# Optimization experiments

Measured on AMD Instinct MI355X. Metric: run time of the kernel, lower is better.

Reference implementation:

```python
import jax, jax.numpy as jnp
import numpy as np

B, S, D, H, L, DFF = 16, 256, 768, 12, 6, 2048
IMG, P, C = 256, 16, 3
HD = D // H
EPS = 1e-5


def _n(k, shp, scale=0.02):
    return jax.random.normal(k, shp, jnp.float32) * scale


def setup_inputs() -> dict:
    key = jax.random.key(0)
    ks = jax.random.split(key, 9)
    return dict(
        encoded_patches=jax.random.normal(ks[0], (B, S, D), jnp.float32),
        W_self_in=_n(ks[1], (L, 3 * D, D)), b_self_in=jnp.zeros((L, 3 * D), jnp.float32),
        W_self_out=_n(ks[2], (L, D, D)), b_self_out=jnp.zeros((L, D), jnp.float32),
        W_cross_in=_n(ks[3], (L, 3 * D, D)), b_cross_in=jnp.zeros((L, 3 * D), jnp.float32),
        W_cross_out=_n(ks[4], (L, D, D)), b_cross_out=jnp.zeros((L, D), jnp.float32),
        ln1_g=jnp.ones((L, D), jnp.float32), ln1_b=jnp.zeros((L, D), jnp.float32),
        ln2_g=jnp.ones((L, D), jnp.float32), ln2_b=jnp.zeros((L, D), jnp.float32),
        ln3_g=jnp.ones((L, D), jnp.float32), ln3_b=jnp.zeros((L, D), jnp.float32),
        W_ff1=_n(ks[5], (L, DFF, D)), b_ff1=jnp.zeros((L, DFF), jnp.float32),
        W_ff2=_n(ks[6], (L, D, DFF)), b_ff2=jnp.zeros((L, D), jnp.float32),
        W_patch=_n(ks[7], (C * P * P, D)), b_patch=jnp.zeros((C * P * P,), jnp.float32),
    )


def sinusoidal_pe(seq, d):
    pos = jnp.arange(seq, dtype=jnp.float32)[:, None]
    div = jnp.exp(jnp.arange(0, d, 2, dtype=jnp.float32) * (-np.log(10000.0) / d))
    pe = jnp.zeros((seq, d), jnp.float32)
    pe = pe.at[:, 0::2].set(jnp.sin(pos * div))
    pe = pe.at[:, 1::2].set(jnp.cos(pos * div))
    return pe


def layer_norm(x, g, b):
    mu = x.mean(-1, keepdims=True)
    var = ((x - mu) ** 2).mean(-1, keepdims=True)
    return (x - mu) * jax.lax.rsqrt(var + EPS) * g + b


def mha(q_in, kv_in, W_in, b_in, W_out, b_out, mask):
    # W_in: [3D, D] packed q,k,v (PyTorch in_proj layout); Linear: y = x W^T + b
    Wq, Wk, Wv = jnp.split(W_in, 3, axis=0)
    bq, bk, bv = jnp.split(b_in, 3, axis=0)
    Bq = q_in.shape[0]
    q = (q_in @ Wq.T + bq).reshape(Bq, -1, H, HD)
    k = (kv_in @ Wk.T + bk).reshape(Bq, -1, H, HD)
    v = (kv_in @ Wv.T + bv).reshape(Bq, -1, H, HD)
    scores = jnp.einsum('bqhd,bkhd->bhqk', q, k) / np.sqrt(HD)
    if mask is not None:
        scores = scores + mask  # mask broadcasts [S, S] with -inf above diag
    attn = jax.nn.softmax(scores, axis=-1)
    out = jnp.einsum('bhqk,bkhd->bqhd', attn, v).reshape(Bq, -1, D)
    return out @ W_out.T + b_out


def reference(encoded_patches, W_self_in, b_self_in, W_self_out, b_self_out,
              W_cross_in, b_cross_in, W_cross_out, b_cross_out,
              ln1_g, ln1_b, ln2_g, ln2_b, ln3_g, ln3_b,
              W_ff1, b_ff1, W_ff2, b_ff2, W_patch, b_patch):
    # The original loops over growing prefixes i=1..S and takes the last
    # position each time. With a causal self-attn mask and per-position
    # cross-attn/FFN/LN, that is mathematically identical to one full
    # causal pass; we compute it once. (eval mode: dropout = identity)
    pe = sinusoidal_pe(S, D)
    causal = jnp.where(jnp.triu(jnp.ones((S, S), jnp.float32), 1) > 0, -jnp.inf, 0.0)
    mem = encoded_patches
    x = encoded_patches + pe[None, :, :]
    for l in range(L):
        # post-norm TransformerDecoderLayer (PyTorch default norm_first=False)
        x = layer_norm(x + mha(x, x, W_self_in[l], b_self_in[l],
                               W_self_out[l], b_self_out[l], causal),
                       ln1_g[l], ln1_b[l])
        x = layer_norm(x + mha(x, mem, W_cross_in[l], b_cross_in[l],
                               W_cross_out[l], b_cross_out[l], None),
                       ln2_g[l], ln2_b[l])
        ff = jax.nn.relu(x @ W_ff1[l].T + b_ff1[l]) @ W_ff2[l].T + b_ff2[l]
        x = layer_norm(x + ff, ln3_g[l], ln3_b[l])
    out = x @ W_patch.T + b_patch                       # [B, S, C*P*P]
    out = out.reshape(-1, IMG, IMG, C)                  # naive view, as in source
    return jnp.transpose(out, (0, 3, 1, 2))             # [B, C, IMG, IMG]
```

## Files before the change

### kernel.cpp

```cpp
#include <hip/hip_runtime.h>
#include <hip/hip_bf16.h>

#define DEV __device__ __forceinline__

typedef __bf16 bf16x8 __attribute__((ext_vector_type(8)));
typedef __bf16 bf16x4 __attribute__((ext_vector_type(4)));
typedef float  f32x4  __attribute__((ext_vector_type(4)));

DEV bf16x8 cvt8(const float4 a, const float4 b) {
    bf16x8 r;
    r[0] = (__bf16)a.x; r[1] = (__bf16)a.y; r[2] = (__bf16)a.z; r[3] = (__bf16)a.w;
    r[4] = (__bf16)b.x; r[5] = (__bf16)b.y; r[6] = (__bf16)b.z; r[7] = (__bf16)b.w;
    return r;
}

DEV void gload_lds16(const __bf16* g, __bf16* l) {
    __builtin_amdgcn_global_load_lds(
        (const __attribute__((address_space(1))) void*)g,
        (__attribute__((address_space(3))) void*)l, 16, 0, 0);
}

DEV void wconv_one(const float* __restrict__ src, __bf16* __restrict__ dst,
                   int lg, int gpr, int K) {
    const int n = lg / gpr;
    const int gi = lg - n * gpr;
    const int cb = (gi >> 3) << 6;
    const int g = gi & 7;
    const float* sp = src + (size_t)n * K + cb + ((g ^ (n & 7)) << 3);
    float4 a = *(const float4*)sp;
    float4 b = *(const float4*)(sp + 4);
    *(bf16x8*)&dst[(size_t)lg * 8] = cvt8(a, b);
}

__global__ __launch_bounds__(256) void wconv(const float* __restrict__ W,
                                             __bf16* __restrict__ Wb) {
    const int gid = blockIdx.x * 256 + threadIdx.x;
    wconv_one(W, Wb, gid, 96, 768);
}

__global__ __launch_bounds__(256) void wconv4(const float* __restrict__ s0,
                                              const float* __restrict__ s1,
                                              const float* __restrict__ s2,
                                              const float* __restrict__ s3,
                                              __bf16* __restrict__ dst) {
    const int gid = blockIdx.x * 256 + threadIdx.x;
    if (gid < 221184)      wconv_one(s0, dst,           gid,          96, 768);
    else if (gid < 294912) wconv_one(s1, dst + 1769472, gid - 221184, 96, 768);
    else if (gid < 516096) wconv_one(s2, dst + 2359296, gid - 294912, 96, 768);
    else                   wconv_one(s3, dst + 4128768, gid - 516096, 96, 768);
}

__global__ __launch_bounds__(256) void wconv_ff(const float* __restrict__ f1,
                                                const float* __restrict__ f2,
                                                __bf16* __restrict__ dst) {
    const int gid = blockIdx.x * 256 + threadIdx.x;
    if (gid < 196608) wconv_one(f1, dst,           gid,          96, 768);
    else              wconv_one(f2, dst + 1572864, gid - 196608, 256, 2048);
}

__global__ __launch_bounds__(256) void cvt_lin(const float* __restrict__ in,
                                               __bf16* __restrict__ out) {
    const int g = blockIdx.x * 256 + threadIdx.x;
    float4 a = *(const float4*)(in + g * 8);
    float4 b = *(const float4*)(in + g * 8 + 4);
    *(bf16x8*)&out[g * 8] = cvt8(a, b);
}

template <int RELU, int OUT_BF16, int BN>
__global__ __launch_bounds__(256) void gemm_bt(const __bf16* __restrict__ Xb,
                                               const __bf16* __restrict__ Wb,
                                               const float* __restrict__ bias,
                                               float* __restrict__ Yf,
                                               __bf16* __restrict__ Yb,
                                               int ldy, int K) {
    __shared__ __bf16 As[128 * 64];
    __shared__ __bf16 Bs[BN * 64];

    const int tid = threadIdx.x;
    const int lane = tid & 63;
    const int wave = tid >> 6;
    constexpr int NI = (BN == 128) ? 4 : 2;
    const int wr = (BN == 128) ? (wave >> 1) : wave;
    const int wc = (BN == 128) ? (wave & 1) : 0;
    const int lr = lane & 15;

    const int mBase = blockIdx.y * 128;
    const int nBase = blockIdx.x * BN;

    const int ar = tid >> 3;
    const int ap = tid & 7;
    const __bf16* Ab = Xb + (size_t)mBase * K + ap * 8;

    const int brow = lane >> 3;
    const __bf16* Bb = Wb + (size_t)nBase * K + (lane & 7) * 8;

    f32x4 acc[NI][4];
#pragma unroll
    for (int i = 0; i < NI; ++i)
#pragma unroll
        for (int j = 0; j < 4; ++j) {
            f32x4 z = {0.f, 0.f, 0.f, 0.f};
            acc[i][j] = z;
        }

    for (int kt = 0; kt < K; kt += 64) {
#pragma unroll
        for (int i = 0; i < 4; ++i) {
            const int row = i * 32 + ar;
            bf16x8 v = *(const bf16x8*)(Ab + (size_t)row * K + kt);
            *(bf16x8*)&As[row * 64 + ((ap ^ (row & 7)) << 3)] = v;
        }
#pragma unroll
        for (int i = 0; i < BN / 32; ++i) {
            const int r0 = wave * (BN / 4) + i * 8;
            gload_lds16(Bb + (size_t)(r0 + brow) * K + kt, &Bs[r0 * 64]);
        }
        __syncthreads();
#pragma unroll
        for (int kk = 0; kk < 2; ++kk) {
            const int q = (lane >> 4) + kk * 4;
            bf16x8 af[NI], bfv[4];
#pragma unroll
            for (int i = 0; i < NI; ++i) {
                const int r = wr * (NI * 16) + i * 16 + lr;
                af[i] = *(const bf16x8*)&As[r * 64 + ((q ^ (r & 7)) << 3)];
            }
#pragma unroll
            for (int j = 0; j < 4; ++j) {
                const int r = wc * 64 + j * 16 + lr;
                bfv[j] = *(const bf16x8*)&Bs[r * 64 + ((q ^ (r & 7)) << 3)];
            }
#pragma unroll
            for (int i = 0; i < NI; ++i)
#pragma unroll
                for (int j = 0; j < 4; ++j)
                    acc[i][j] = __builtin_amdgcn_mfma_f32_16x16x32_bf16(af[i], bfv[j], acc[i][j], 0, 0, 0);
        }
        __syncthreads();
    }

    const int rsub = (lane >> 4) << 2;
#pragma unroll
    for (int i = 0; i < NI; ++i)
#pragma unroll
        for (int j = 0; j < 4; ++j) {
            const int col = nBase + wc * 64 + j * 16 + lr;
            const float bv = bias[col];
#pragma unroll
            for (int rr = 0; rr < 4; ++rr) {
                const int row = mBase + wr * (NI * 16) + i * 16 + rsub + rr;
                float v = acc[i][j][rr] + bv;
                if (RELU) v = fmaxf(v, 0.f);
                if (OUT_BF16) Yb[(size_t)row * ldy + col] = (__bf16)v;
                else          Yf[(size_t)row * ldy + col] = v;
            }
        }
}

__global__ __launch_bounds__(256) void attn_mfma(const __bf16* __restrict__ QKV,
                                                 __bf16* __restrict__ Oout,
                                                 int causal) {
    const int bh = blockIdx.x;
    const int qq = blockIdx.y;
    const int b = bh / 12, h = bh - b * 12;
    const int tid = threadIdx.x;
    const int lane = tid & 63;
    const int w = tid >> 6;
    const int g = lane >> 4;
    const int c = lane & 15;
    const int c7 = c & 7;

    __shared__ __bf16 Ks[64 * 64];
    __shared__ __bf16 Vs[64 * 66];
    __shared__ __bf16 Ps[64 * 64];

    const int q64 = (w << 4) + c;
    const int qrow = (qq << 6) + q64;
    const __bf16* qp = QKV + (size_t)((b << 8) + qrow) * 2304 + (h << 6) + (g << 3);
    bf16x8 qf0 = *(const bf16x8*)qp;
    bf16x8 qf1 = *(const bf16x8*)(qp + 32);

    f32x4 oacc[4];
#pragma unroll
    for (int i = 0; i < 4; ++i) { f32x4 z = {0.f, 0.f, 0.f, 0.f}; oacc[i] = z; }
    float mrun = -1e30f, lrun = 0.f;

    const int nt = causal ? (qq + 1) : 4;
    const int sr = tid >> 2;
    const int sg0 = (tid & 3) << 1;
    const int sp = sg0 << 3;

    for (int kt = 0; kt < nt; ++kt) {
        __syncthreads();
        {
            const __bf16* kp = QKV + (size_t)((b << 8) + (kt << 6) + sr) * 2304 + 768 + (h << 6) + sp;
            bf16x8 k0 = *(const bf16x8*)kp;
            bf16x8 k1 = *(const bf16x8*)(kp + 8);
            bf16x8 v0 = *(const bf16x8*)(kp + 768);
            bf16x8 v1 = *(const bf16x8*)(kp + 776);
            const int s7 = sr & 7;
            *(bf16x8*)&Ks[(sr << 6) + ((sg0 ^ s7) << 3)] = k0;
            *(bf16x8*)&Ks[(sr << 6) + (((sg0 + 1) ^ s7) << 3)] = k1;
            uint32_t* vd = (uint32_t*)&Vs[sr * 66 + sp];
            const uint32_t* u0 = (const uint32_t*)&v0;
            const uint32_t* u1 = (const uint32_t*)&v1;
            vd[0] = u0[0]; vd[1] = u0[1]; vd[2] = u0[2]; vd[3] = u0[3];
            vd[4] = u1[0]; vd[5] = u1[1]; vd[6] = u1[2]; vd[7] = u1[3];
        }
        __syncthreads();

        f32x4 sc[4];
#pragma unroll
        for (int mf = 0; mf < 4; ++mf) { f32x4 z = {0.f, 0.f, 0.f, 0.f}; sc[mf] = z; }
#pragma unroll
        for (int mf = 0; mf < 4; ++mf) {
            const int row = (mf << 4) + c;
            bf16x8 af0 = *(const bf16x8*)&Ks[(row << 6) + ((g ^ c7) << 3)];
            sc[mf] = __builtin_amdgcn_mfma_f32_16x16x32_bf16(af0, qf0, sc[mf], 0, 0, 0);
            bf16x8 af1 = *(const bf16x8*)&Ks[(row << 6) + (((g + 4) ^ c7) << 3)];
            sc[mf] = __builtin_amdgcn_mfma_f32_16x16x32_bf16(af1, qf1, sc[mf], 0, 0, 0);
        }

        const int diag = (causal && kt == qq);
        float tm = -1e30f;
#pragma unroll
        for (int mf = 0; mf < 4; ++mf)
#pragma unroll
            for (int r = 0; r < 4; ++r) {
                float v = sc[mf][r] * 0.125f;
                if (diag && ((mf << 4) + (g << 2) + r > q64)) v = -1e30f;
                sc[mf][r] = v;
                tm = fmaxf(tm, v);
            }
        tm = fmaxf(tm, __shfl_xor(tm, 16));
        tm = fmaxf(tm, __shfl_xor(tm, 32));
        const float mnew = fmaxf(mrun, tm);
        const float rs = __expf(mrun - mnew);
        mrun = mnew;
        lrun *= rs;
#pragma unroll
        for (int i = 0; i < 4; ++i) {
            oacc[i][0] *= rs; oacc[i][1] *= rs; oacc[i][2] *= rs; oacc[i][3] *= rs;
        }

#pragma unroll
        for (int mf = 0; mf < 4; ++mf) {
            const int kg = (mf << 1) + (g >> 1);
            const int e = (g & 1) << 2;
#pragma unroll
            for (int r = 0; r < 4; ++r) {
                float p = __expf(sc[mf][r] - mnew);
                lrun += p;
                Ps[(q64 << 6) + ((kg ^ c7) << 3) + e + r] = (__bf16)p;
            }
        }

#pragma unroll
        for (int kc = 0; kc < 2; ++kc) {
            bf16x8 pb = *(const bf16x8*)&Ps[(q64 << 6) + (((g + (kc << 2)) ^ c7) << 3)];
#pragma unroll
            for (int df = 0; df < 4; ++df) {
                bf16x8 av;
#pragma unroll
                for (int j = 0; j < 8; ++j)
                    av[j] = Vs[((g << 3) + j + (kc << 5)) * 66 + (df << 4) + c];
                oacc[df] = __builtin_amdgcn_mfma_f32_16x16x32_bf16(av, pb, oacc[df], 0, 0, 0);
            }
        }
    }

    lrun += __shfl_xor(lrun, 16);
    lrun += __shfl_xor(lrun, 32);
    const float inv = 1.f / lrun;
    __bf16* op = Oout + (size_t)((b << 8) + qrow) * 768 + (h << 6) + (g << 2);
#pragma unroll
    for (int df = 0; df < 4; ++df) {
        bf16x4 ov;
        ov[0] = (__bf16)(oacc[df][0] * inv);
        ov[1] = (__bf16)(oacc[df][1] * inv);
        ov[2] = (__bf16)(oacc[df][2] * inv);
        ov[3] = (__bf16)(oacc[df][3] * inv);
        *(bf16x4*)(op + (df << 4)) = ov;
    }
}

__global__ __launch_bounds__(256) void resid_ln(float* __restrict__ x,
                                                __bf16* __restrict__ xb,
                                                const float* __restrict__ r,
                                                const float* __restrict__ g,
                                                const float* __restrict__ b) {
    const int row = blockIdx.x, tid = threadIdx.x;
    float* xp = x + (size_t)row * 768;
    __bf16* xbp = xb + (size_t)row * 768;
    const float* rp = r + (size_t)row * 768;

    float v0 = xp[tid] + rp[tid];
    float v1 = xp[tid + 256] + rp[tid + 256];
    float v2 = xp[tid + 512] + rp[tid + 512];

    __shared__ float red[4];
    float s = v0 + v1 + v2;
#pragma unroll
    for (int off = 32; off > 0; off >>= 1) s += __shfl_down(s, off, 64);
    if ((tid & 63) == 0) red[tid >> 6] = s;
    __syncthreads();
    const float mean = (red[0] + red[1] + red[2] + red[3]) * (1.0f / 768.0f);
    __syncthreads();

    float d0 = v0 - mean, d1 = v1 - mean, d2 = v2 - mean;
    float q = d0 * d0 + d1 * d1 + d2 * d2;
#pragma unroll
    for (int off = 32; off > 0; off >>= 1) q += __shfl_down(q, off, 64);
    if ((tid & 63) == 0) red[tid >> 6] = q;
    __syncthreads();
    const float inv = rsqrtf((red[0] + red[1] + red[2] + red[3]) * (1.0f / 768.0f) + 1e-5f);

    const float o0 = d0 * inv * g[tid] + b[tid];
    const float o1 = d1 * inv * g[tid + 256] + b[tid + 256];
    const float o2 = d2 * inv * g[tid + 512] + b[tid + 512];
    xp[tid] = o0;       xbp[tid] = (__bf16)o0;
    xp[tid + 256] = o1; xbp[tid + 256] = (__bf16)o1;
    xp[tid + 512] = o2; xbp[tid + 512] = (__bf16)o2;
}

__global__ __launch_bounds__(256) void add_pe(const float* __restrict__ e,
                                              float* __restrict__ x,
                                              __bf16* __restrict__ xb) {
    const int i = blockIdx.x * 256 + threadIdx.x;
    const int m = i / 768;
    const int d = i - m * 768;
    const int s = m & 255;
    const int pair = d >> 1;
    const float div = __expf((float)(2 * pair) * (-0.011992630693328381f));
    const float ang = (float)s * div;
    const float pe = (d & 1) ? cosf(ang) : sinf(ang);
    const float v = e[i] + pe;
    x[i] = v;
    xb[i] = (__bf16)v;
}

__global__ __launch_bounds__(256) void write_out(const float* __restrict__ p, float* __restrict__ o) {
    const int i = blockIdx.x * 256 + threadIdx.x;
    const int m = i / 768;
    const int j = i - m * 768;
    const int b = m >> 8, s = m & 255;
    const int w = j / 3;
    const int c = j - w * 3;
    o[(size_t)b * 196608 + (size_t)c * 65536 + s * 256 + w] = p[i];
}

extern "C" void kernel_launch(void* const* d_in, const int* in_sizes, int n_in,
                              void* d_out, int out_size, void* d_ws, size_t ws_size,
                              hipStream_t stream) {
    const float* enc         = (const float*)d_in[0];
    const float* W_self_in   = (const float*)d_in[1];
    const float* b_self_in   = (const float*)d_in[2];
    const float* W_self_out  = (const float*)d_in[3];
    const float* b_self_out  = (const float*)d_in[4];
    const float* W_cross_in  = (const float*)d_in[5];
    const float* b_cross_in  = (const float*)d_in[6];
    const float* W_cross_out = (const float*)d_in[7];
    const float* b_cross_out = (const float*)d_in[8];
    const float* ln1_g       = (const float*)d_in[9];
    const float* ln1_b       = (const float*)d_in[10];
    const float* ln2_g       = (const float*)d_in[11];
    const float* ln2_b       = (const float*)d_in[12];
    const float* ln3_g       = (const float*)d_in[13];
    const float* ln3_b       = (const float*)d_in[14];
    const float* W_ff1       = (const float*)d_in[15];
    const float* b_ff1       = (const float*)d_in[16];
    const float* W_ff2       = (const float*)d_in[17];
    const float* b_ff2       = (const float*)d_in[18];
    const float* W_patch     = (const float*)d_in[19];
    const float* b_patch     = (const float*)d_in[20];

    float* out = (float*)d_out;
    float* ws  = (float*)d_ws;

    float*  x       = ws;
    __bf16* xb      = (__bf16*)(ws + 3145728);
    __bf16* qkvb    = (__bf16*)(ws + 4718592);
    __bf16* attnout = (__bf16*)(ws + 9437184);
    float*  proj    = ws + 11010048;
    __bf16* encb    = (__bf16*)(ws + 14155776);
    __bf16* wbuf    = (__bf16*)(ws + 15728640);

    add_pe<<<12288, 256, 0, stream>>>(enc, x, xb);
    cvt_lin<<<1536, 256, 0, stream>>>(enc, encb);

    for (int l = 0; l < 6; ++l) {
        const float* Wsi = W_self_in   + (size_t)l * 2304 * 768;
        const float* Wso = W_self_out  + (size_t)l * 768 * 768;
        const float* Wci = W_cross_in  + (size_t)l * 2304 * 768;
        const float* Wco = W_cross_out + (size_t)l * 768 * 768;
        const float* Wf1 = W_ff1       + (size_t)l * 2048 * 768;
        const float* Wf2 = W_ff2       + (size_t)l * 768 * 2048;

        wconv4<<<2304, 256, 0, stream>>>(Wsi, Wso, Wci, Wco, wbuf);

        gemm_bt<0, 1, 128><<<dim3(18, 32), 256, 0, stream>>>(xb, wbuf, b_self_in + l * 2304,
                                                             nullptr, qkvb, 2304, 768);
        attn_mfma<<<dim3(192, 4), 256, 0, stream>>>(qkvb, attnout, 1);
        gemm_bt<0, 0, 64><<<dim3(12, 32), 256, 0, stream>>>(attnout, wbuf + 1769472,
                                                            b_self_out + l * 768,
                                                            proj, nullptr, 768, 768);
        resid_ln<<<4096, 256, 0, stream>>>(x, xb, proj, ln1_g + l * 768, ln1_b + l * 768);

        gemm_bt<0, 1, 64><<<dim3(12, 32), 256, 0, stream>>>(xb, wbuf + 2359296,
                                                            b_cross_in + l * 2304,
                                                            nullptr, qkvb, 2304, 768);
        gemm_bt<0, 1, 128><<<dim3(12, 32), 256, 0, stream>>>(encb, wbuf + 2949120,
                                                             b_cross_in + l * 2304 + 768,
                                                             nullptr, qkvb + 768, 2304, 768);
        attn_mfma<<<dim3(192, 4), 256, 0, stream>>>(qkvb, attnout, 0);
        gemm_bt<0, 0, 64><<<dim3(12, 32), 256, 0, stream>>>(attnout, wbuf + 4128768,
                                                            b_cross_out + l * 768,
                                                            proj, nullptr, 768, 768);
        resid_ln<<<4096, 256, 0, stream>>>(x, xb, proj, ln2_g + l * 768, ln2_b + l * 768);

        wconv_ff<<<1536, 256, 0, stream>>>(Wf1, Wf2, wbuf);
        gemm_bt<1, 1, 128><<<dim3(16, 32), 256, 0, stream>>>(xb, wbuf, b_ff1 + l * 2048,
                                                             nullptr, qkvb, 2048, 768);
        gemm_bt<0, 0, 64><<<dim3(12, 32), 256, 0, stream>>>(qkvb, wbuf + 1572864,
                                                            b_ff2 + l * 768,
                                                            proj, nullptr, 768, 2048);
        resid_ln<<<4096, 256, 0, stream>>>(x, xb, proj, ln3_g + l * 768, ln3_b + l * 768);
    }

    wconv<<<288, 256, 0, stream>>>(W_patch, wbuf);
    gemm_bt<0, 0, 64><<<dim3(12, 32), 256, 0, stream>>>(xb, wbuf, b_patch,
                                                        proj, nullptr, 768, 768);
    write_out<<<12288, 256, 0, stream>>>(proj, out);
}
```

Measured before the change: 1.486 ms.

## Pre-swizzle bf16 activations so GEMM A-tiles load directly into LDS

Producers of bf16 activations (layer norm, embedding, GEMM bf16 epilogue, attention output) now write rows in the XOR-swizzled layout the GEMM expects. The GEMM can then load A tiles with direct global-to-LDS loads, and attention can load K the same way. The change also remaps block IDs across 8 groups for cache locality, fuses the enc conversion into add_pe, vectorises add_pe with fast sin/cos, and writes the final output permutation straight from the GEMM epilogue, removing the write_out kernel. The risk is that every consumer must agree on the swizzle, and the fast sin/cos intrinsics lower accuracy slightly.

```diff
diff --git a/kernel.cpp b/kernel.cpp
--- a/kernel.cpp
+++ b/kernel.cpp
@@ -18,6 +18,10 @@
     __builtin_amdgcn_global_load_lds(
         (const __attribute__((address_space(1))) void*)g,
         (__attribute__((address_space(3))) void*)l, 16, 0, 0);
+}
+
+DEV int swzcol(int col, int row) {
+    return (col & ~63) | ((((col >> 3) & 7) ^ (row & 7)) << 3) | (col & 7);
 }
 
 DEV void wconv_one(const float* __restrict__ src, __bf16* __restrict__ dst,
@@ -58,15 +62,7 @@
     else              wconv_one(f2, dst + 1572864, gid - 196608, 256, 2048);
 }
 
-__global__ __launch_bounds__(256) void cvt_lin(const float* __restrict__ in,
-                                               __bf16* __restrict__ out) {
-    const int g = blockIdx.x * 256 + threadIdx.x;
-    float4 a = *(const float4*)(in + g * 8);
-    float4 b = *(const float4*)(in + g * 8 + 4);
-    *(bf16x8*)&out[g * 8] = cvt8(a, b);
-}
-
-template <int RELU, int OUT_BF16, int BN>
+template <int RELU, int OUT, int BN>
 __global__ __launch_bounds__(256) void gemm_bt(const __bf16* __restrict__ Xb,
                                                const __bf16* __restrict__ Wb,
                                                const float* __restrict__ bias,
@@ -84,15 +80,18 @@
     const int wc = (BN == 128) ? (wave & 1) : 0;
     const int lr = lane & 15;
 
-    const int mBase = blockIdx.y * 128;
-    const int nBase = blockIdx.x * BN;
-
-    const int ar = tid >> 3;
-    const int ap = tid & 7;
-    const __bf16* Ab = Xb + (size_t)mBase * K + ap * 8;
+    const int nx = gridDim.x;
+    int bid = blockIdx.y * nx + blockIdx.x;
+    const int cpx = (nx * gridDim.y) >> 3;
+    bid = (bid & 7) * cpx + (bid >> 3);
+    const int by = bid / nx;
+    const int bx = bid - by * nx;
+    const int mBase = by * 128;
+    const int nBase = bx * BN;
 
     const int brow = lane >> 3;
-    const __bf16* Bb = Wb + (size_t)nBase * K + (lane & 7) * 8;
+    const __bf16* Ap = Xb + (size_t)mBase * K + ((lane & 7) << 3);
+    const __bf16* Bp = Wb + (size_t)nBase * K + ((lane & 7) << 3);
 
     f32x4 acc[NI][4];
 #pragma unroll
@@ -106,29 +105,28 @@
     for (int kt = 0; kt < K; kt += 64) {
 #pragma unroll
         for (int i = 0; i < 4; ++i) {
-            const int row = i * 32 + ar;
-            bf16x8 v = *(const bf16x8*)(Ab + (size_t)row * K + kt);
-            *(bf16x8*)&As[row * 64 + ((ap ^ (row & 7)) << 3)] = v;
+            const int r0 = (wave << 5) + (i << 3);
+            gload_lds16(Ap + (size_t)(r0 + brow) * K + kt, &As[r0 << 6]);
         }
 #pragma unroll
         for (int i = 0; i < BN / 32; ++i) {
-            const int r0 = wave * (BN / 4) + i * 8;
-            gload_lds16(Bb + (size_t)(r0 + brow) * K + kt, &Bs[r0 * 64]);
+            const int r0 = wave * (BN / 4) + (i << 3);
+            gload_lds16(Bp + (size_t)(r0 + brow) * K + kt, &Bs[r0 << 6]);
         }
         __syncthreads();
 #pragma unroll
         for (int kk = 0; kk < 2; ++kk) {
-            const int q = (lane >> 4) + kk * 4;
+            const int q = (lane >> 4) + (kk << 2);
             bf16x8 af[NI], bfv[4];
 #pragma unroll
             for (int i = 0; i < NI; ++i) {
                 const int r = wr * (NI * 16) + i * 16 + lr;
-                af[i] = *(const bf16x8*)&As[r * 64 + ((q ^ (r & 7)) << 3)];
+                af[i] = *(const bf16x8*)&As[(r << 6) + ((q ^ (r & 7)) << 3)];
             }
 #pragma unroll
             for (int j = 0; j < 4; ++j) {
                 const int r = wc * 64 + j * 16 + lr;
-                bfv[j] = *(const bf16x8*)&Bs[r * 64 + ((q ^ (r & 7)) << 3)];
+                bfv[j] = *(const bf16x8*)&Bs[(r << 6) + ((q ^ (r & 7)) << 3)];
             }
 #pragma unroll
             for (int i = 0; i < NI; ++i)
@@ -151,8 +149,15 @@
                 const int row = mBase + wr * (NI * 16) + i * 16 + rsub + rr;
                 float v = acc[i][j][rr] + bv;
                 if (RELU) v = fmaxf(v, 0.f);
-                if (OUT_BF16) Yb[(size_t)row * ldy + col] = (__bf16)v;
-                else          Yf[(size_t)row * ldy + col] = v;
+                if (OUT == 1) {
+                    Yb[(size_t)row * ldy + swzcol(col, row)] = (__bf16)v;
+                } else if (OUT == 2) {
+                    const int b_ = row >> 8, s_ = row & 255;
+                    const int w_ = col / 3, c_ = col - w_ * 3;
+                    Yf[(size_t)b_ * 196608 + (size_t)c_ * 65536 + s_ * 256 + w_] = v;
+                } else {
+                    Yf[(size_t)row * ldy + col] = v;
+                }
             }
         }
 }
@@ -172,13 +177,12 @@
 
     __shared__ __bf16 Ks[64 * 64];
     __shared__ __bf16 Vs[64 * 66];
-    __shared__ __bf16 Ps[64 * 64];
 
     const int q64 = (w << 4) + c;
     const int qrow = (qq << 6) + q64;
-    const __bf16* qp = QKV + (size_t)((b << 8) + qrow) * 2304 + (h << 6) + (g << 3);
-    bf16x8 qf0 = *(const bf16x8*)qp;
-    bf16x8 qf1 = *(const bf16x8*)(qp + 32);
+    const __bf16* qp = QKV + (size_t)((b << 8) + qrow) * 2304 + (h << 6);
+    bf16x8 qf0 = *(const bf16x8*)(qp + ((g ^ c7) << 3));
+    bf16x8 qf1 = *(const bf16x8*)(qp + (((g + 4) ^ c7) << 3));
 
     f32x4 oacc[4];
 #pragma unroll
@@ -193,19 +197,24 @@
     for (int kt = 0; kt < nt; ++kt) {
         __syncthreads();
         {
-            const __bf16* kp = QKV + (size_t)((b << 8) + (kt << 6) + sr) * 2304 + 768 + (h << 6) + sp;
-            bf16x8 k0 = *(const bf16x8*)kp;
-            bf16x8 k1 = *(const bf16x8*)(kp + 8);
-            bf16x8 v0 = *(const bf16x8*)(kp + 768);
-            bf16x8 v1 = *(const bf16x8*)(kp + 776);
+            const __bf16* Kp = QKV + (size_t)((b << 8) + (kt << 6)) * 2304 + 768 + (h << 6) + ((lane & 7) << 3);
+#pragma unroll
+            for (int i = 0; i < 2; ++i) {
+                const int r0 = (w << 4) + (i << 3);
+                gload_lds16(Kp + (size_t)(r0 + (lane >> 3)) * 2304, &Ks[r0 << 6]);
+            }
+        }
+        {
+            const __bf16* vp = QKV + (size_t)((b << 8) + (kt << 6) + sr) * 2304 + 1536 + (h << 6);
+            bf16x8 v0 = *(const bf16x8*)(vp + sp);
+            bf16x8 v1 = *(const bf16x8*)(vp + sp + 8);
             const int s7 = sr & 7;
-            *(bf16x8*)&Ks[(sr << 6) + ((sg0 ^ s7) << 3)] = k0;
-            *(bf16x8*)&Ks[(sr << 6) + (((sg0 + 1) ^ s7) << 3)] = k1;
-            uint32_t* vd = (uint32_t*)&Vs[sr * 66 + sp];
+            uint32_t* d0 = (uint32_t*)&Vs[sr * 66 + ((sg0 ^ s7) << 3)];
+            uint32_t* d1 = (uint32_t*)&Vs[sr * 66 + (((sg0 + 1) ^ s7) << 3)];
             const uint32_t* u0 = (const uint32_t*)&v0;
             const uint32_t* u1 = (const uint32_t*)&v1;
-            vd[0] = u0[0]; vd[1] = u0[1]; vd[2] = u0[2]; vd[3] = u0[3];
-            vd[4] = u1[0]; vd[5] = u1[1]; vd[6] = u1[2]; vd[7] = u1[3];
+            d0[0] = u0[0]; d0[1] = u0[1]; d0[2] = u0[2]; d0[3] = u0[3];
+            d1[0] = u1[0]; d1[1] = u1[1]; d1[2] = u1[2]; d1[3] = u1[3];
         }
         __syncthreads();
 
@@ -243,6 +252,7 @@
             oacc[i][0] *= rs; oacc[i][1] *= rs; oacc[i][2] *= rs; oacc[i][3] *= rs;
         }
 
+        __shared__ __bf16 Ps[64 * 64];
 #pragma unroll
         for (int mf = 0; mf < 4; ++mf) {
             const int kg = (mf << 1) + (g >> 1);
@@ -272,7 +282,7 @@
     lrun += __shfl_xor(lrun, 16);
     lrun += __shfl_xor(lrun, 32);
     const float inv = 1.f / lrun;
-    __bf16* op = Oout + (size_t)((b << 8) + qrow) * 768 + (h << 6) + (g << 2);
+    __bf16* op = Oout + (size_t)((b << 8) + qrow) * 768 + (h << 6);
 #pragma unroll
     for (int df = 0; df < 4; ++df) {
         bf16x4 ov;
@@ -280,7 +290,8 @@
         ov[1] = (__bf16)(oacc[df][1] * inv);
         ov[2] = (__bf16)(oacc[df][2] * inv);
         ov[3] = (__bf16)(oacc[df][3] * inv);
-        *(bf16x4*)(op + (df << 4)) = ov;
+        const int gran = (df << 1) + (g >> 1);
+        *(bf16x4*)(op + ((gran ^ c7) << 3) + ((g & 1) << 2)) = ov;
     }
 }
 
@@ -318,35 +329,43 @@
     const float o0 = d0 * inv * g[tid] + b[tid];
     const float o1 = d1 * inv * g[tid + 256] + b[tid + 256];
     const float o2 = d2 * inv * g[tid + 512] + b[tid + 512];
-    xp[tid] = o0;       xbp[tid] = (__bf16)o0;
-    xp[tid + 256] = o1; xbp[tid + 256] = (__bf16)o1;
-    xp[tid + 512] = o2; xbp[tid + 512] = (__bf16)o2;
+    xp[tid] = o0;       xbp[swzcol(tid, row)] = (__bf16)o0;
+    xp[tid + 256] = o1; xbp[swzcol(tid + 256, row)] = (__bf16)o1;
+    xp[tid + 512] = o2; xbp[swzcol(tid + 512, row)] = (__bf16)o2;
 }
 
 __global__ __launch_bounds__(256) void add_pe(const float* __restrict__ e,
                                               float* __restrict__ x,
-                                              __bf16* __restrict__ xb) {
-    const int i = blockIdx.x * 256 + threadIdx.x;
-    const int m = i / 768;
-    const int d = i - m * 768;
+                                              __bf16* __restrict__ xb,
+                                              __bf16* __restrict__ encb) {
+    const int gid = blockIdx.x * 256 + threadIdx.x;
+    const int m = gid / 96;
+    const int g8 = gid - m * 96;
+    const int col0 = g8 << 3;
     const int s = m & 255;
-    const int pair = d >> 1;
-    const float div = __expf((float)(2 * pair) * (-0.011992630693328381f));
-    const float ang = (float)s * div;
-    const float pe = (d & 1) ? cosf(ang) : sinf(ang);
-    const float v = e[i] + pe;
-    x[i] = v;
-    xb[i] = (__bf16)v;
-}
-
-__global__ __launch_bounds__(256) void write_out(const float* __restrict__ p, float* __restrict__ o) {
-    const int i = blockIdx.x * 256 + threadIdx.x;
-    const int m = i / 768;
-    const int j = i - m * 768;
-    const int b = m >> 8, s = m & 255;
-    const int w = j / 3;
-    const int c = j - w * 3;
-    o[(size_t)b * 196608 + (size_t)c * 65536 + s * 256 + w] = p[i];
+
+    float4 e0 = *(const float4*)(e + (size_t)m * 768 + col0);
+    float4 e1 = *(const float4*)(e + (size_t)m * 768 + col0 + 4);
+
+    float pe[8];
+#pragma unroll
+    for (int p = 0; p < 4; ++p) {
+        const int d = col0 + 2 * p;
+        const float div = __expf((float)d * (-0.011992630693328381f));
+        const float ang = (float)s * div;
+        pe[2 * p] = __sinf(ang);
+        pe[2 * p + 1] = __cosf(ang);
+    }
+    float4 v0, v1;
+    v0.x = e0.x + pe[0]; v0.y = e0.y + pe[1]; v0.z = e0.z + pe[2]; v0.w = e0.w + pe[3];
+    v1.x = e1.x + pe[4]; v1.y = e1.y + pe[5]; v1.z = e1.z + pe[6]; v1.w = e1.w + pe[7];
+
+    *(float4*)(x + (size_t)m * 768 + col0) = v0;
+    *(float4*)(x + (size_t)m * 768 + col0 + 4) = v1;
+
+    const int scb = (col0 & ~63) | ((((g8 & 7) ^ (m & 7)) << 3));
+    *(bf16x8*)&xb[(size_t)m * 768 + scb] = cvt8(v0, v1);
+    *(bf16x8*)&encb[(size_t)m * 768 + scb] = cvt8(e0, e1);
 }
 
 extern "C" void kernel_launch(void* const* d_in, const int* in_sizes, int n_in,
@@ -385,8 +404,7 @@
     __bf16* encb    = (__bf16*)(ws + 14155776);
     __bf16* wbuf    = (__bf16*)(ws + 15728640);
 
-    add_pe<<<12288, 256, 0, stream>>>(enc, x, xb);
-    cvt_lin<<<1536, 256, 0, stream>>>(enc, encb);
+    add_pe<<<1536, 256, 0, stream>>>(enc, x, xb, encb);
 
     for (int l = 0; l < 6; ++l) {
         const float* Wsi = W_self_in   + (size_t)l * 2304 * 768;
@@ -428,7 +446,6 @@
     }
 
     wconv<<<288, 256, 0, stream>>>(W_patch, wbuf);
-    gemm_bt<0, 0, 64><<<dim3(12, 32), 256, 0, stream>>>(xb, wbuf, b_patch,
-                                                        proj, nullptr, 768, 768);
-    write_out<<<12288, 256, 0, stream>>>(proj, out);
-}
+    gemm_bt<0, 2, 64><<<dim3(12, 32), 256, 0, stream>>>(xb, wbuf, b_patch,
+                                                        out, nullptr, 768, 768);
+}
```

Result: faster. 1.450 ms (-2.4%).
